# Kernel optimization log

Hardware: AMD Instinct MI355X
Metric: run time of the kernel (lower is better)

## Reference

```python
import math
import jax, jax.numpy as jnp
import numpy as np

B, S, HIDDEN = 1, 8192, 2048
NUM_HEADS = 16
HEAD_DIM = HIDDEN // NUM_HEADS
NUM_FW = 4
FW_DIM = HIDDEN // NUM_FW
D_H = FW_DIM  # inter_multi = 1.0
WINDOW = 256
CHUNK = 2048
ROPE_THETA = 500000.0
BASE_LR_INV = float(np.log(np.expm1(0.001)))  # inv_softplus(1e-3)


def rms_norm(x, w, eps=1e-6):
    return x * jax.lax.rsqrt(jnp.mean(x * x, axis=-1, keepdims=True) + eps) * w


def apply_rope(q, k, theta):
    D = q.shape[-1]
    inv = 1.0 / (theta ** (jnp.arange(0, D, 2, dtype=jnp.float32) / D))
    t = jnp.arange(q.shape[1], dtype=jnp.float32)
    f = t[:, None] * inv[None, :]  # [S, D/2]
    cos = jnp.cos(f)[None, :, None, :]
    sin = jnp.sin(f)[None, :, None, :]
    def ap(x):
        x1, x2 = jnp.split(x, 2, axis=-1)
        return jnp.concatenate([x1 * cos - x2 * sin, x2 * cos + x1 * sin], axis=-1)
    return ap(q), ap(k)


def sliding_window_attn(q, k, v, window):
    # q,k,v: [B,S,H,D]; causal window of `window` tokens incl. self (flash (window-1, 0))
    B_, S_, H_, D_ = q.shape
    W = window
    nc = S_ // W
    def blk(x):
        return x.transpose(0, 2, 1, 3).reshape(B_, H_, nc, W, D_)
    qb, kb, vb = blk(q), blk(k), blk(v)
    pad = jnp.zeros((B_, H_, 1, W, D_), q.dtype)
    k2 = jnp.concatenate([jnp.concatenate([pad, kb[:, :, :-1]], 2), kb], 3)  # [B,H,nc,2W,D]
    v2 = jnp.concatenate([jnp.concatenate([pad, vb[:, :, :-1]], 2), vb], 3)
    r = jnp.arange(W)[:, None]
    j = jnp.arange(2 * W)[None, :]
    base = (j >= r + 1) & (j <= W + r)  # causal + within-window
    keypos = (jnp.arange(nc)[:, None, None] - 1) * W + j[None]
    mask = base[None] & (keypos >= 0)  # [nc,W,2W]
    scores = jnp.einsum('bhnqd,bhnkd->bhnqk', qb, k2) * (1.0 / math.sqrt(D_))
    scores = jnp.where(mask[None, None], scores, -jnp.inf)
    p = jax.nn.softmax(scores, axis=-1)
    o = jnp.einsum('bhnqk,bhnkd->bhnqd', p, v2)
    return o.reshape(B_, H_, S_, D_).transpose(0, 2, 1, 3)


def ttt_swiglu(fq, fk, fv, l0, l1, l2, w0, w1, w2, chunk):
    # fq/fk/fv: [BN,S,d]; l*: [BN,S,1]; w0,w2: [BN,dh,d]; w1: [BN,d,dh]
    BN, S_, d = fq.shape
    nc = S_ // chunk
    def ch(x):
        return x.reshape(BN, nc, chunk, x.shape[-1]).transpose(1, 0, 2, 3)
    xs = (ch(fq), ch(fk), ch(fv), ch(l0), ch(l1), ch(l2))
    def step(carry, x):
        w0c, w1c, w2c = carry
        qi, ki, vi, lr0, lr1, lr2 = x
        # apply current fast weights to chunk queries (SwiGLU MLP)
        o = jnp.einsum('bch,boh->bco',
                       jax.nn.silu(jnp.einsum('bcd,bhd->bch', qi, w0c)) * jnp.einsum('bcd,bhd->bch', qi, w2c),
                       w1c)
        # manual gradient of dot-product TTT loss L = -sum(v * f(k))
        g = jnp.einsum('bcd,bhd->bch', ki, w0c)
        hm = jnp.einsum('bcd,bhd->bch', ki, w2c)
        sg = jax.nn.sigmoid(g)
        silu_g = g * sg
        hid = silu_g * hm
        dhid = jnp.einsum('bco,boh->bch', vi, w1c)
        dhm = dhid * silu_g
        dg = dhid * hm
        dgp = dg * (sg * (1.0 + g * (1.0 - sg)))  # silu backprop
        w0n = w0c + jnp.einsum('bch,bcd->bhd', dgp * lr0, ki)
        w2n = w2c + jnp.einsum('bch,bcd->bhd', dhm * lr2, ki)
        w1n = w1c + jnp.einsum('bco,bch->boh', vi * lr1, hid)
        return (w0n, w1n, w2n), o
    _, outs = jax.lax.scan(step, (w0, w1, w2), xs)
    return outs.transpose(1, 0, 2, 3).reshape(BN, S_, d)


def setup_inputs():
    key = jax.random.key(0)
    ks = jax.random.split(key, 8)
    h = HIDDEN
    return {
        'hidden_states': jax.random.normal(ks[0], (B, S, h), jnp.float32),
        'qkv_w': jax.random.normal(ks[1], (3 * h, h), jnp.float32) * 0.02,
        'q_norm_w': jnp.ones((h,), jnp.float32),
        'k_norm_w': jnp.ones((h,), jnp.float32),
        'qk_scale': jnp.ones((h, 2), jnp.float32),
        'qk_offset': jnp.zeros((h, 2), jnp.float32),
        'lr_w': jax.random.normal(ks[2], (3 * NUM_FW, h), jnp.float32) * 0.02,
        'lr_b': jnp.zeros((3 * NUM_FW,), jnp.float32),
        'w0': jax.random.normal(ks[3], (NUM_FW, D_H, FW_DIM), jnp.float32) / math.sqrt(FW_DIM),
        'w1': jax.random.normal(ks[4], (NUM_FW, FW_DIM, D_H), jnp.float32) / math.sqrt(D_H),
        'w2': jax.random.normal(ks[5], (NUM_FW, D_H, FW_DIM), jnp.float32) / math.sqrt(FW_DIM),
        'ttt_norm_w': jnp.ones((FW_DIM,), jnp.float32),
        'o_proj_w': jax.random.normal(ks[6], (h, h), jnp.float32) * 0.02,
    }


def reference(hidden_states, qkv_w, q_norm_w, k_norm_w, qk_scale, qk_offset,
              lr_w, lr_b, w0, w1, w2, ttt_norm_w, o_proj_w):
    qkv = hidden_states @ qkv_w.T
    q, k, v = jnp.split(qkv, 3, axis=-1)
    q = rms_norm(q, q_norm_w)
    k = rms_norm(k, k_norm_w)
    # rescale q/k for the fast-weight path
    fq = q * qk_scale[:, 0] + qk_offset[:, 0]
    fk = k * qk_scale[:, 1] + qk_offset[:, 1]
    fv = v
    # windowed RoPE attention path
    qh = q.reshape(B, S, NUM_HEADS, HEAD_DIM)
    kh = k.reshape(B, S, NUM_HEADS, HEAD_DIM)
    vh = v.reshape(B, S, NUM_HEADS, HEAD_DIM)
    qh, kh = apply_rope(qh, kh, ROPE_THETA)
    attn_o = sliding_window_attn(qh, kh, vh, WINDOW).reshape(B, S, HIDDEN)
    # fast-weight (TTT) path: silu + per-head l2-norm on q/k
    fq = jax.nn.silu(fq).reshape(B, S, NUM_FW, FW_DIM)
    fk = jax.nn.silu(fk).reshape(B, S, NUM_FW, FW_DIM)
    fv = jax.nn.silu(fv).reshape(B, S, NUM_FW, FW_DIM)
    fq = fq / jnp.maximum(jnp.linalg.norm(fq, axis=-1, keepdims=True), 1e-12)
    fk = fk / jnp.maximum(jnp.linalg.norm(fk, axis=-1, keepdims=True), 1e-12)
    def flat(x):
        return x.transpose(0, 2, 1, 3).reshape(B * NUM_FW, S, FW_DIM)
    # per-token learning rates (mamba parameterization)
    lr = jax.nn.softplus(hidden_states @ lr_w.T + lr_b + BASE_LR_INV)  # [B,S,3*NH]
    l0, l1, l2 = jnp.split(lr, 3, axis=-1)
    def flat_lr(x):
        return x.transpose(0, 2, 1).reshape(B * NUM_FW, S, 1)
    def bcast(w):
        return jnp.broadcast_to(w[None], (B,) + w.shape).reshape(B * NUM_FW, w.shape[1], w.shape[2])
    o_fast = ttt_swiglu(flat(fq), flat(fk), flat(fv),
                        flat_lr(l0), flat_lr(l1), flat_lr(l2),
                        bcast(w0), bcast(w1), bcast(w2), CHUNK)
    o_fast = rms_norm(o_fast.reshape(B, NUM_FW, S, FW_DIM), ttt_norm_w)
    o_fast = o_fast.transpose(0, 2, 1, 3).reshape(B, S, HIDDEN)
    return (attn_o + o_fast) @ o_proj_w.T
```

## Files before the change

### kernel.cpp

```cpp
#include <hip/hip_runtime.h>
#include <hip/hip_bf16.h>

typedef __hip_bfloat16 bf16;
typedef __bf16 bft;
typedef bft bf16x8 __attribute__((ext_vector_type(8)));
typedef bft bf16x4 __attribute__((ext_vector_type(4)));
typedef float f32x4 __attribute__((ext_vector_type(4)));

#define S_LEN 8192
#define HID   2048
#define QKV3  6144
#define NH    16
#define HD    128
#define NFW   4
#define FD    512
#define CHUNK_LEN 2048
#define NCHUNK 4
#define BASE_LR_INV (-6.9072552f)
#define QKP 136
#define VSP 72
#define PSP 76

__device__ __forceinline__ float bf2f(bf16 x){ return __bfloat162float(x); }
__device__ __forceinline__ bf16  f2bf(float x){ return __float2bfloat16(x); }
__device__ __forceinline__ float sigm(float x){ return 1.f/(1.f+__expf(-x)); }
__device__ __forceinline__ float siluf(float x){ return x/(1.f+__expf(-x)); }
__device__ __forceinline__ float wave_sum(float v){
  #pragma unroll
  for(int off=32; off; off>>=1) v += __shfl_xor(v, off, 64);
  return v;
}

template<int N>
__device__ __forceinline__ void waitcnt_vm(){
  static_assert(N==0||N==2||N==4||N==8, "unsupported vmcnt");
  if constexpr (N==0)      asm volatile("s_waitcnt vmcnt(0)" ::: "memory");
  else if constexpr (N==2) asm volatile("s_waitcnt vmcnt(2)" ::: "memory");
  else if constexpr (N==4) asm volatile("s_waitcnt vmcnt(4)" ::: "memory");
  else                     asm volatile("s_waitcnt vmcnt(8)" ::: "memory");
}

__device__ __forceinline__ void bar(){
  __builtin_amdgcn_s_barrier();
  asm volatile("" ::: "memory");
}

template<int ROWS>
__device__ __forceinline__ void stage(const bft* __restrict__ src, long ld,
                                      bft* dst, int tid)
{
  const int lane = tid & 63, wv = tid >> 6;
  #pragma unroll
  for (int i = 0; i < ROWS/64; ++i) {
    const int r0 = wv*16 + i*64;
    const int row = r0 + (lane >> 2);
    const int g = (lane & 3) ^ ((row >> 1) & 3);
    const bft* gp = src + (size_t)row*ld + g*8;
    bft* lp = dst + (size_t)r0*32;
    __builtin_amdgcn_global_load_lds(
        (const __attribute__((address_space(1))) void*)gp,
        (__attribute__((address_space(3))) void*)lp, 16, 0, 0);
  }
}

template<int BM,int BN,int EPI>
__global__ __launch_bounds__(256) void mgemm_k(
    const bft* __restrict__ A, const bft* __restrict__ B, void* __restrict__ Cv,
    bft* __restrict__ Cd, bft* __restrict__ Ct, int K,
    long lda, long ldb, long ldc, long sA, long sB, long sC, long sCd)
{
  constexpr int AM = BM/32, AN = BN/32;
  constexpr int LPT = BM/64 + BN/64;
  constexpr int NPH = (AM >= 4) ? 2 : 1;
  constexpr int MH  = AM / NPH;
  __shared__ __align__(16) bft As[4][BM*32];
  __shared__ __align__(16) bft Bs[4][BN*32];
  const int tid = threadIdx.x;
  const int z = blockIdx.z;
  A += (size_t)z * sA;
  B += (size_t)z * sB;
  const size_t m0 = (size_t)blockIdx.y * BM, n0 = (size_t)blockIdx.x * BN;
  const int wv = tid >> 6, lane = tid & 63;
  const int wm = (wv & 1) * (BM/2), wn = (wv >> 1) * (BN/2);
  const int fr = lane & 15;
  const int fsw = ((lane >> 4) ^ ((fr >> 1) & 3)) * 8;

  f32x4 acc[AM][AN];
  #pragma unroll
  for (int i=0;i<AM;i++)
    #pragma unroll
    for (int j=0;j<AN;j++) acc[i][j] = (f32x4){0.f,0.f,0.f,0.f};

  const bft* Ab = A + m0*lda;
  const bft* Bb = B + n0*ldb;
  const int NS = K >> 5;

  stage<BM>(Ab,      lda, As[0], tid);
  stage<BN>(Bb,      ldb, Bs[0], tid);
  stage<BM>(Ab + 32, lda, As[1], tid);
  stage<BN>(Bb + 32, ldb, Bs[1], tid);
  waitcnt_vm<LPT>();
  bar();

  for (int s = 0; s < NS; ++s) {
    const bft* Ap = As[s & 3];
    const bft* Bp = Bs[s & 3];
    const int kt = (s + 2) * 32;
    const bool st = (s + 2 < NS);

    bf16x8 bvv[AN], afv[MH];
    #pragma unroll
    for (int ni=0; ni<AN; ni++)
      bvv[ni] = *(const bf16x8*)(Bp + (size_t)(wn + ni*16 + fr)*32 + fsw);
    #pragma unroll
    for (int i=0; i<MH; i++)
      afv[i] = *(const bf16x8*)(Ap + (size_t)(wm + i*16 + fr)*32 + fsw);
    if (st) stage<BM>(Ab + kt, lda, As[(s+2)&3], tid);
    if constexpr (NPH == 1) {
      if (st) { stage<BN>(Bb + kt, ldb, Bs[(s+2)&3], tid); waitcnt_vm<LPT>(); }
      else waitcnt_vm<0>();
    }
    bar();
    __builtin_amdgcn_s_setprio(1);
    #pragma unroll
    for (int i=0; i<MH; i++)
      #pragma unroll
      for (int ni=0; ni<AN; ni++)
        acc[i][ni] = __builtin_amdgcn_mfma_f32_16x16x32_bf16(afv[i], bvv[ni], acc[i][ni], 0, 0, 0);
    __builtin_amdgcn_s_setprio(0);

    if constexpr (NPH == 2) {
      bar();
      #pragma unroll
      for (int i=0; i<MH; i++)
        afv[i] = *(const bf16x8*)(Ap + (size_t)(wm + (MH+i)*16 + fr)*32 + fsw);
      if (st) { stage<BN>(Bb + kt, ldb, Bs[(s+2)&3], tid); waitcnt_vm<LPT>(); }
      else waitcnt_vm<0>();
      bar();
      __builtin_amdgcn_s_setprio(1);
      #pragma unroll
      for (int i=0; i<MH; i++)
        #pragma unroll
        for (int ni=0; ni<AN; ni++)
          acc[MH+i][ni] = __builtin_amdgcn_mfma_f32_16x16x32_bf16(afv[i], bvv[ni], acc[MH+i][ni], 0, 0, 0);
      __builtin_amdgcn_s_setprio(0);
      bar();
    }
  }

  const int er = (lane >> 4) * 4;
  const int ec = lane & 15;
  #pragma unroll
  for (int mi=0; mi<AM; mi++){
    #pragma unroll
    for (int ni=0; ni<AN; ni++){
      #pragma unroll
      for (int r=0; r<4; r++){
        size_t row = m0 + wm + mi*16 + er + r;
        size_t col = n0 + wn + ni*16 + ec;
        size_t idx = (size_t)z*sC + row*ldc + col;
        float v = acc[mi][ni][r];
        if constexpr (EPI == 0){
          ((bft*)Cv)[idx] = (bft)v;
        } else if constexpr (EPI == 1){
          ((float*)Cv)[idx] = v;
        } else {
          float nv = ((float*)Cv)[idx] + v;
          ((float*)Cv)[idx] = nv;
          Cd[(size_t)z*sCd + row*ldc + col] = (bft)nv;
          if (Ct) Ct[(size_t)z*FD*FD + col*FD + row] = (bft)nv;
        }
      }
    }
  }
}

template<int BM,int BN,int EPI>
static inline void mgemm(hipStream_t st, const bft* A, const bft* B, void* C,
    bft* Cd, bft* Ct, int M, int N, int K, long lda, long ldb, long ldc,
    int batch, long sA, long sB, long sC, long sCd)
{
  dim3 g(N/BN, M/BM, batch);
  mgemm_k<BM,BN,EPI><<<g, 256, 0, st>>>(A, B, C, Cd, Ct, K, lda, ldb, ldc, sA, sB, sC, sCd);
}

__device__ __forceinline__ void stage8(const bft* __restrict__ src, long ld,
                                       bft* dst, int tid)
{
  const int lane = tid & 63, wv = tid >> 6;
  #pragma unroll
  for (int i = 0; i < 2; ++i) {
    const int r0 = wv*16 + i*128;
    const int row = r0 + (lane >> 2);
    const int g = (lane & 3) ^ ((row >> 1) & 3);
    const bft* gp = src + (size_t)row*ld + g*8;
    bft* lp = dst + (size_t)r0*32;
    __builtin_amdgcn_global_load_lds(
        (const __attribute__((address_space(1))) void*)gp,
        (__attribute__((address_space(3))) void*)lp, 16, 0, 0);
  }
}

#define M8_ROW(mi, a) { \
    acc[mi][0]=__builtin_amdgcn_mfma_f32_16x16x32_bf16(a,bv[0],acc[mi][0],0,0,0); \
    acc[mi][1]=__builtin_amdgcn_mfma_f32_16x16x32_bf16(a,bv[1],acc[mi][1],0,0,0); \
    acc[mi][2]=__builtin_amdgcn_mfma_f32_16x16x32_bf16(a,bv[2],acc[mi][2],0,0,0); \
    acc[mi][3]=__builtin_amdgcn_mfma_f32_16x16x32_bf16(a,bv[3],acc[mi][3],0,0,0); }

template<int EPI>
__global__ __launch_bounds__(512, 2) void mgemm8_k(
    const bft* __restrict__ A, const bft* __restrict__ B, void* __restrict__ Cv,
    int K, long lda, long ldb, long ldc)
{
  __shared__ __align__(16) bft As[4][256*32];
  __shared__ __align__(16) bft Bs[4][256*32];
  const int tid = threadIdx.x;

  const int gx = (int)gridDim.x;
  const int nwg = (int)(gridDim.x * gridDim.y);
  int lin = (int)(blockIdx.y * gridDim.x + blockIdx.x);
  if ((nwg & 7) == 0) lin = (lin & 7) * (nwg >> 3) + (lin >> 3);
  const size_t m0 = (size_t)(lin / gx) * 256;
  const size_t n0 = (size_t)(lin % gx) * 256;

  const int wv = tid >> 6, lane = tid & 63;
  const int wm = (wv & 1) * 128, wn = (wv >> 1) * 64;
  const int fr = lane & 15;
  const int fsw = ((lane >> 4) ^ ((fr >> 1) & 3)) * 8;

  f32x4 acc[8][4];
  #pragma unroll
  for (int i=0;i<8;i++)
    #pragma unroll
    for (int j=0;j<4;j++) acc[i][j] = (f32x4){0.f,0.f,0.f,0.f};

  const bft* Ab = A + m0*lda;
  const bft* Bb = B + n0*ldb;
  const int NS = K >> 5;

  stage8(Ab,      lda, As[0], tid);
  stage8(Bb,      ldb, Bs[0], tid);
  stage8(Ab + 32, lda, As[1], tid);
  stage8(Bb + 32, ldb, Bs[1], tid);
  waitcnt_vm<4>();
  bar();

  for (int s = 0; s < NS; ++s) {
    const bft* Ap = As[s & 3];
    const bft* Bp = Bs[s & 3];
    const int kt = (s + 2) * 32;
    const bool st = (s + 2 < NS);
    bf16x8 bv[4], a0, a1, a2, a3;

    bv[0] = *(const bf16x8*)(Bp + (size_t)(wn +  0 + fr)*32 + fsw);
    bv[1] = *(const bf16x8*)(Bp + (size_t)(wn + 16 + fr)*32 + fsw);
    bv[2] = *(const bf16x8*)(Bp + (size_t)(wn + 32 + fr)*32 + fsw);
    bv[3] = *(const bf16x8*)(Bp + (size_t)(wn + 48 + fr)*32 + fsw);
    a0 = *(const bf16x8*)(Ap + (size_t)(wm +  0 + fr)*32 + fsw);
    a1 = *(const bf16x8*)(Ap + (size_t)(wm + 16 + fr)*32 + fsw);
    a2 = *(const bf16x8*)(Ap + (size_t)(wm + 32 + fr)*32 + fsw);
    a3 = *(const bf16x8*)(Ap + (size_t)(wm + 48 + fr)*32 + fsw);
    if (st) stage8(Ab + kt, lda, As[(s+2)&3], tid);
    bar();
    __builtin_amdgcn_s_setprio(1);
    M8_ROW(0, a0); M8_ROW(1, a1); M8_ROW(2, a2); M8_ROW(3, a3);
    __builtin_amdgcn_s_setprio(0);
    bar();

    a0 = *(const bf16x8*)(Ap + (size_t)(wm +  64 + fr)*32 + fsw);
    a1 = *(const bf16x8*)(Ap + (size_t)(wm +  80 + fr)*32 + fsw);
    a2 = *(const bf16x8*)(Ap + (size_t)(wm +  96 + fr)*32 + fsw);
    a3 = *(const bf16x8*)(Ap + (size_t)(wm + 112 + fr)*32 + fsw);
    if (st) { stage8(Bb + kt, ldb, Bs[(s+2)&3], tid); waitcnt_vm<4>(); }
    else waitcnt_vm<0>();
    bar();
    __builtin_amdgcn_s_setprio(1);
    M8_ROW(4, a0); M8_ROW(5, a1); M8_ROW(6, a2); M8_ROW(7, a3);
    __builtin_amdgcn_s_setprio(0);
    bar();
  }

  const int er = (lane >> 4) * 4;
  const int ec = lane & 15;
  #pragma unroll
  for (int mi=0; mi<8; mi++){
    #pragma unroll
    for (int ni=0; ni<4; ni++){
      #pragma unroll
      for (int r=0; r<4; r++){
        size_t row = m0 + wm + mi*16 + er + r;
        size_t col = n0 + wn + ni*16 + ec;
        size_t idx = row*ldc + col;
        float v = acc[mi][ni][r];
        if constexpr (EPI == 0) ((bft*)Cv)[idx] = (bft)v;
        else                    ((float*)Cv)[idx] = v;
      }
    }
  }
}

template<int EPI>
static inline void mgemm8(hipStream_t st, const bft* A, const bft* B, void* C,
                          int M, int N, int K, long lda, long ldb, long ldc)
{
  dim3 g(N/256, M/256, 1);
  mgemm8_k<EPI><<<g, 512, 0, st>>>(A, B, C, K, lda, ldb, ldc);
}

__global__ __launch_bounds__(256) void cvt_k(const float* __restrict__ s,
    bft* __restrict__ d)
{
  size_t i = ((size_t)blockIdx.x*256 + threadIdx.x) * 8;
  const float4 v0 = *(const float4*)(s + i);
  const float4 v1 = *(const float4*)(s + i + 4);
  bf16x8 b;
  b[0]=(bft)v0.x; b[1]=(bft)v0.y; b[2]=(bft)v0.z; b[3]=(bft)v0.w;
  b[4]=(bft)v1.x; b[5]=(bft)v1.y; b[6]=(bft)v1.z; b[7]=(bft)v1.w;
  *(bf16x8*)(d + i) = b;
}

__global__ __launch_bounds__(256) void tr_k(const bft* __restrict__ in,
    bft* __restrict__ out, long ldin, long sIn, long sOut)
{
  __shared__ __align__(16) bft t[64][72];
  const int c0 = blockIdx.x*64, r0 = blockIdx.y*64;
  in  += (size_t)blockIdx.z * sIn;
  out += (size_t)blockIdx.z * sOut;
  const int tid = threadIdx.x;
  #pragma unroll
  for (int i=0;i<2;i++){
    int e = tid + i*256;
    int r = e >> 3, c8 = (e & 7) * 8;
    *(bf16x8*)&t[r][c8] = *(const bf16x8*)(in + (size_t)(r0+r)*ldin + c0 + c8);
  }
  __syncthreads();
  #pragma unroll
  for (int i=0;i<2;i++){
    int e = tid + i*256;
    int c = e >> 3, r8 = (e & 7) * 8;
    bf16x8 v;
    #pragma unroll
    for (int j=0;j<8;j++) v[j] = t[r8+j][c];
    *(bf16x8*)(out + (size_t)(c0+c)*CHUNK_LEN + r0 + r8) = v;
  }
}

__global__ __launch_bounds__(256) void tcw1_k(const float* __restrict__ w1,
    bft* __restrict__ w1tb)
{
  size_t idx = (size_t)blockIdx.x*256 + threadIdx.x;
  int z = (int)(idx >> 18);
  int h = (int)((idx >> 9) & 511);
  int o = (int)(idx & 511);
  w1tb[idx] = (bft)w1[(size_t)z*FD*FD + (size_t)o*FD + h];
}

__global__ __launch_bounds__(256) void vt_k(const bf16* __restrict__ qkv,
    bft* __restrict__ vT)
{
  __shared__ __align__(16) bft t[64*QKP];
  const int s0 = blockIdx.x * 64;
  const int h  = blockIdx.y;
  const int tid = threadIdx.x;
  #pragma unroll
  for (int i=0;i<4;i++){
    int e = tid + i*256;
    int rr = e >> 4, doff = (e & 15) * 8;
    *(bf16x8*)(t + rr*QKP + doff) =
        *(const bf16x8*)((const bft*)qkv + (size_t)(s0+rr)*QKV3 + 2*HID + h*HD + doff);
  }
  __syncthreads();
  #pragma unroll
  for (int it=0; it<4; it++){
    int d = (tid >> 3) + it*32;
    int so8 = (tid & 7) * 8;
    bf16x8 v;
    #pragma unroll
    for (int j=0;j<8;j++) v[j] = t[(so8+j)*QKP + d];
    *(bf16x8*)(vT + ((size_t)(h*HD + d))*S_LEN + s0 + so8) = v;
  }
}

__global__ void rope_k(float* __restrict__ rc, float* __restrict__ rs){
  int pos = blockIdx.x, d = threadIdx.x;
  float inv = 1.f / powf(500000.0f, (float)d * (1.0f/64.0f));
  float ang = (float)pos * inv;
  rc[pos*64+d] = cosf(ang);
  rs[pos*64+d] = sinf(ang);
}

__global__ __launch_bounds__(256) void lr_k(const float* __restrict__ hidden,
    const float* __restrict__ lr_w, const float* __restrict__ lr_b,
    float* __restrict__ lro)
{
  __shared__ float hrow[HID];
  __shared__ float red[4][12];
  int s = blockIdx.x, tid = threadIdx.x;
  for(int i=0;i<HID/256;i++) hrow[tid+256*i] = hidden[(size_t)s*HID + tid + 256*i];
  __syncthreads();
  float part[12];
  #pragma unroll
  for(int o=0;o<12;o++) part[o]=0.f;
  for(int i=0;i<HID/256;i++){
    int j = tid + 256*i;
    float h = hrow[j];
    #pragma unroll
    for(int o=0;o<12;o++) part[o] += h * lr_w[o*HID + j];
  }
  int lane = tid & 63, w = tid >> 6;
  #pragma unroll
  for(int o=0;o<12;o++){
    float v = wave_sum(part[o]);
    if(lane==0) red[w][o] = v;
  }
  __syncthreads();
  if(tid < 12){
    float v = red[0][tid]+red[1][tid]+red[2][tid]+red[3][tid] + lr_b[tid] + BASE_LR_INV;
    float sp = (v > 20.f) ? v : log1pf(expf(v));
    lro[s*12 + tid] = sp;
  }
}

__global__ __launch_bounds__(256) void e2a_k(
    bf16* __restrict__ qkv,
    const float* __restrict__ qnw, const float* __restrict__ knw)
{
  __shared__ float red[8];
  int s = blockIdx.x, tid = threadIdx.x;
  int lane = tid & 63, w = tid >> 6;
  float qv[8], kv[8];
  float sq = 0.f, sk = 0.f;
  size_t base = (size_t)s*QKV3;
  #pragma unroll
  for(int i=0;i<8;i++){
    int j = tid*8 + i;
    qv[i] = bf2f(qkv[base + j]);
    kv[i] = bf2f(qkv[base + HID + j]);
    sq += qv[i]*qv[i]; sk += kv[i]*kv[i];
  }
  sq = wave_sum(sq); sk = wave_sum(sk);
  if(lane==0){ red[w] = sq; red[4+w] = sk; }
  __syncthreads();
  float rq = rsqrtf((red[0]+red[1]+red[2]+red[3])*(1.f/HID) + 1e-6f);
  float rk = rsqrtf((red[4]+red[5]+red[6]+red[7])*(1.f/HID) + 1e-6f);
  #pragma unroll
  for(int i=0;i<8;i++){
    int j = tid*8 + i;
    qkv[base + j]       = f2bf(qv[i]*rq*qnw[j]);
    qkv[base + HID + j] = f2bf(kv[i]*rk*knw[j]);
  }
}

__global__ __launch_bounds__(256) void e2b_k(
    bf16* __restrict__ qkv,
    const float* __restrict__ qks, const float* __restrict__ qko)
{
  int s = blockIdx.x, tid = threadIdx.x;
  size_t base = (size_t)s*QKV3;
  float a[8], b[8], vv[8];
  float ga = 0.f, gb2 = 0.f;
  #pragma unroll
  for(int i=0;i<8;i++){
    int j = tid*8 + i;
    float qn = bf2f(qkv[base + j]);
    float kn = bf2f(qkv[base + HID + j]);
    float v  = bf2f(qkv[base + 2*HID + j]);
    a[i] = siluf(qn*qks[2*j]   + qko[2*j]);
    b[i] = siluf(kn*qks[2*j+1] + qko[2*j+1]);
    vv[i] = siluf(v);
    ga += a[i]*a[i]; gb2 += b[i]*b[i];
  }
  ga = wave_sum(ga); gb2 = wave_sum(gb2);
  float iq = 1.f / fmaxf(sqrtf(ga), 1e-12f);
  float ik = 1.f / fmaxf(sqrtf(gb2), 1e-12f);
  #pragma unroll
  for(int i=0;i<8;i++){
    int j = tid*8 + i;
    qkv[base + j]         = f2bf(a[i]*iq);
    qkv[base + HID + j]   = f2bf(b[i]*ik);
    qkv[base + 2*HID + j] = f2bf(vv[i]);
  }
}

__global__ __launch_bounds__(256) void attn_k(
    const bf16* __restrict__ qkv, const bft* __restrict__ vT,
    const float* __restrict__ rc, const float* __restrict__ rs,
    float* __restrict__ attn)
{
  __shared__ __align__(16) bft Qs[64*QKP];
  __shared__ __align__(16) bft Ks[64*QKP];
  __shared__ __align__(16) bft Vs[128*VSP];
  __shared__ __align__(16) bft Ps[64*PSP];
  const int head = blockIdx.x >> 7;
  const int Q0 = (blockIdx.x & 127) * 64;
  const int tid = threadIdx.x;
  const int hb = head * HD;
  const int lane = tid & 63;
  const int wm = (tid >> 6) * 16;
  const int fr = lane & 15, fko = (lane >> 4) * 8;
  const int rbase = (lane >> 4) * 4;

  #pragma unroll
  for(int i=0;i<16;i++){
    int e = tid + i*256;
    int rr = e >> 6, d = e & 63;
    int qpos = Q0 + rr;
    size_t b = (size_t)qpos*QKV3 + hb;
    float x1 = bf2f(qkv[b + d]);
    float x2 = bf2f(qkv[b + d + 64]);
    float c = rc[qpos*64 + d], sn = rs[qpos*64 + d];
    Qs[rr*QKP + d]      = (bft)(x1*c - x2*sn);
    Qs[rr*QKP + d + 64] = (bft)(x2*c + x1*sn);
  }
  __syncthreads();
  bf16x8 qf[4];
  #pragma unroll
  for (int kk=0;kk<4;kk++)
    qf[kk] = *(const bf16x8*)(Qs + (wm+fr)*QKP + kk*32 + fko);

  f32x4 Ot[8];
  #pragma unroll
  for (int i=0;i<8;i++) Ot[i] = (f32x4){0.f,0.f,0.f,0.f};
  float m4[4], l4[4];
  #pragma unroll
  for (int r=0;r<4;r++){ m4[r] = -INFINITY; l4[r] = 0.f; }

  for (int kt=0; kt<5; kt++){
    const int kb = Q0 - 256 + kt*64;
    if (kb < 0) continue;
    __syncthreads();
    #pragma unroll
    for(int i=0;i<16;i++){
      int e = tid + i*256;
      int rr = e >> 6, d = e & 63;
      int kpos = kb + rr;
      size_t b = (size_t)kpos*QKV3 + HID + hb;
      float x1 = bf2f(qkv[b + d]);
      float x2 = bf2f(qkv[b + d + 64]);
      float c = rc[kpos*64 + d], sn = rs[kpos*64 + d];
      Ks[rr*QKP + d]      = (bft)(x1*c - x2*sn);
      Ks[rr*QKP + d + 64] = (bft)(x2*c + x1*sn);
    }
    {
      int d = tid >> 1, koff = (tid & 1) * 32;
      const bft* vrow = vT + ((size_t)(hb + d))*S_LEN + kb + koff;
      bft* lrow = Vs + d*VSP + koff;
      #pragma unroll
      for (int j8=0;j8<4;j8++)
        *(bf16x8*)(lrow + j8*8) = *(const bf16x8*)(vrow + j8*8);
    }
    __syncthreads();

    f32x4 st[4];
    #pragma unroll
    for (int nt=0;nt<4;nt++){
      f32x4 acc = (f32x4){0.f,0.f,0.f,0.f};
      #pragma unroll
      for (int kk=0;kk<4;kk++){
        bf16x8 kf = *(const bf16x8*)(Ks + (nt*16+fr)*QKP + kk*32 + fko);
        acc = __builtin_amdgcn_mfma_f32_16x16x32_bf16(qf[kk], kf, acc, 0, 0, 0);
      }
      st[nt] = acc;
    }

    float pv[4][4];
    #pragma unroll
    for (int r=0;r<4;r++){
      int qpos = Q0 + wm + rbase + r;
      float sm[4];
      float mx = -INFINITY;
      #pragma unroll
      for (int nt=0;nt<4;nt++){
        int kpos = kb + nt*16 + fr;
        bool valid = (kpos > qpos - 256) && (kpos <= qpos);
        float s = valid ? st[nt][r] * 0.088388347648318447f : -INFINITY;
        sm[nt] = s;
        mx = fmaxf(mx, s);
      }
      mx = fmaxf(mx, __shfl_xor(mx, 1, 64));
      mx = fmaxf(mx, __shfl_xor(mx, 2, 64));
      mx = fmaxf(mx, __shfl_xor(mx, 4, 64));
      mx = fmaxf(mx, __shfl_xor(mx, 8, 64));
      float mnew = fmaxf(m4[r], mx);
      float alpha = (mnew == -INFINITY) ? 1.f : __expf(m4[r] - mnew);
      float ps = 0.f;
      #pragma unroll
      for (int nt=0;nt<4;nt++){
        float p = (sm[nt] == -INFINITY) ? 0.f : __expf(sm[nt] - mnew);
        pv[nt][r] = p;
        ps += p;
      }
      ps += __shfl_xor(ps, 1, 64);
      ps += __shfl_xor(ps, 2, 64);
      ps += __shfl_xor(ps, 4, 64);
      ps += __shfl_xor(ps, 8, 64);
      l4[r] = l4[r]*alpha + ps;
      m4[r] = mnew;
      #pragma unroll
      for (int ct=0;ct<8;ct++) Ot[ct][r] *= alpha;
    }

    #pragma unroll
    for (int r=0;r<4;r++){
      int row = wm + rbase + r;
      #pragma unroll
      for (int nt=0;nt<4;nt++)
        Ps[row*PSP + nt*16 + fr] = (bft)pv[nt][r];
    }
    bf16x8 af[2];
    #pragma unroll
    for (int kk=0;kk<2;kk++){
      const bft* pp = Ps + (wm+fr)*PSP + kk*32 + fko;
      bf16x4 lo = *(const bf16x4*)pp;
      bf16x4 hi = *(const bf16x4*)(pp+4);
      bf16x8 a;
      #pragma unroll
      for (int j=0;j<4;j++){ a[j]=lo[j]; a[j+4]=hi[j]; }
      af[kk]=a;
    }
    #pragma unroll
    for (int ct=0;ct<8;ct++)
      #pragma unroll
      for (int kk=0;kk<2;kk++){
        bf16x8 bv = *(const bf16x8*)(Vs + (ct*16+fr)*VSP + kk*32 + fko);
        Ot[ct] = __builtin_amdgcn_mfma_f32_16x16x32_bf16(af[kk], bv, Ot[ct], 0, 0, 0);
      }
  }

  #pragma unroll
  for (int r=0;r<4;r++){
    float invl = 1.f / l4[r];
    int qpos = Q0 + wm + rbase + r;
    size_t ob = (size_t)qpos*HID + hb;
    #pragma unroll
    for (int ct=0;ct<8;ct++)
      attn[ob + ct*16 + fr] = Ot[ct][r] * invl;
  }
}

__global__ __launch_bounds__(256) void e3f_k(
    bft* __restrict__ gh, bft* __restrict__ qgm, bft* __restrict__ hid)
{
  size_t idx = (size_t)blockIdx.x*256 + threadIdx.x;
  int z  = (int)(idx >> 20);
  int ci = (int)((idx >> 9) & 2047);
  int d  = (int)(idx & 511);
  size_t b = ((size_t)z*CHUNK_LEN + ci)*1024 + d;
  float opre = siluf((float)qgm[b]) * (float)qgm[b + 512];
  hid[idx] = (bft)(siluf((float)gh[b]) * (float)gh[b + 512]);
  qgm[b]   = (bft)opre;
}

__global__ __launch_bounds__(256) void e4f_k(
    bft* __restrict__ gh, bft* __restrict__ qgm,
    const bf16* __restrict__ qkv, const float* __restrict__ lrb, int cbase)
{
  size_t idx = (size_t)blockIdx.x*256 + threadIdx.x;
  int z  = (int)(idx >> 20);
  int ci = (int)((idx >> 9) & 2047);
  int d  = (int)(idx & 511);
  int s  = cbase + ci;
  float l0  = lrb[s*12 + z];
  float l1  = lrb[s*12 + 4 + z];
  float l2v = lrb[s*12 + 8 + z];
  size_t b = ((size_t)z*CHUNK_LEN + ci)*1024 + d;
  float gg = (float)gh[b], hv = (float)gh[b + 512], dh = (float)qgm[b + 512];
  float sg = sigm(gg);
  float silu_g = gg * sg;
  float dhm = dh * silu_g;
  float dg  = dh * hv;
  float dgp = dg * (sg * (1.f + gg * (1.f - sg)));
  float fvv = bf2f(qkv[(size_t)s*QKV3 + 2*HID + z*FD + d]);
  gh[b]        = (bft)(dgp * l0);
  gh[b + 512]  = (bft)(dhm * l2v);
  qgm[b + 512] = (bft)(fvv * l1);
}

__global__ __launch_bounds__(256) void e5_k(const float* __restrict__ attn,
    const bf16* __restrict__ ofc, const float* __restrict__ tnw,
    bf16* __restrict__ qkv, int cbase)
{
  int ci = blockIdx.x, tid = threadIdx.x;
  int s = cbase + ci;
  int lane = tid & 63, w = tid >> 6;
  float o[8]; float ss = 0.f;
  size_t ob = ((size_t)w*CHUNK_LEN + ci)*FD + (size_t)lane*8;
  #pragma unroll
  for(int i=0;i<8;i++){ o[i] = bf2f(ofc[ob+i]); ss += o[i]*o[i]; }
  ss = wave_sum(ss);
  float inv = rsqrtf(ss*(1.f/FD) + 1e-6f);
  size_t xb = (size_t)s*QKV3 + w*FD + (size_t)lane*8;
  size_t ab = (size_t)s*HID  + w*FD + (size_t)lane*8;
  #pragma unroll
  for(int i=0;i<8;i++){
    int d = lane*8 + i;
    qkv[xb+i] = f2bf(attn[ab+i] + o[i]*inv*tnw[d]);
  }
}

extern "C" void kernel_launch(void* const* d_in, const int* in_sizes, int n_in,
                              void* d_out, int out_size, void* d_ws, size_t ws_size,
                              hipStream_t stream)
{
  (void)in_sizes; (void)n_in; (void)out_size;
  const float* hidden   = (const float*)d_in[0];
  const float* qkv_w    = (const float*)d_in[1];
  const float* q_norm_w = (const float*)d_in[2];
  const float* k_norm_w = (const float*)d_in[3];
  const float* qk_scale = (const float*)d_in[4];
  const float* qk_off   = (const float*)d_in[5];
  const float* lr_w     = (const float*)d_in[6];
  const float* lr_b     = (const float*)d_in[7];
  const float* w0_in    = (const float*)d_in[8];
  const float* w1_in    = (const float*)d_in[9];
  const float* w2_in    = (const float*)d_in[10];
  const float* ttt_nw   = (const float*)d_in[11];
  const float* o_proj   = (const float*)d_in[12];
  float* out = (float*)d_out;

  char* p = (char*)d_ws;
  auto alloc = [&](size_t n){ char* r = p; p += (n + 255) & ~(size_t)255; return (void*)r; };

  bf16*  qkv   = (bf16*) alloc((size_t)S_LEN*QKV3*sizeof(bf16));
  float* lrb   = (float*)alloc((size_t)S_LEN*12*sizeof(float));
  float* rc    = (float*)alloc((size_t)S_LEN*64*sizeof(float));
  float* rs    = (float*)alloc((size_t)S_LEN*64*sizeof(float));
  float* w0s   = (float*)alloc((size_t)NFW*FD*FD*sizeof(float));
  float* w1s   = (float*)alloc((size_t)NFW*FD*FD*sizeof(float));
  float* w2s   = (float*)alloc((size_t)NFW*FD*FD*sizeof(float));
  bft*   w1tb  = (bft*)  alloc((size_t)NFW*FD*FD*sizeof(bft));
  bft*   w02b  = (bft*)  alloc((size_t)NFW*1024*FD*sizeof(bft));
  bft*   w1b   = (bft*)  alloc((size_t)NFW*FD*FD*sizeof(bft));
  bf16*  gb    = (bf16*) alloc((size_t)NFW*CHUNK_LEN*FD*sizeof(bf16));
  bf16*  hmb   = (bf16*) alloc((size_t)NFW*CHUNK_LEN*FD*sizeof(bf16));
  bf16*  qgb   = (bf16*) alloc((size_t)NFW*CHUNK_LEN*FD*sizeof(bf16));
  bf16*  qmb   = (bf16*) alloc((size_t)NFW*CHUNK_LEN*FD*sizeof(bf16));
  bf16*  hidb  = (bf16*) alloc((size_t)NFW*CHUNK_LEN*FD*sizeof(bf16));
  bf16*  ofc   = (bf16*) alloc((size_t)NFW*CHUNK_LEN*FD*sizeof(bf16));
  bft*   fkT   = (bft*)  alloc((size_t)NFW*FD*CHUNK_LEN*sizeof(bft));
  bft*   hidT  = (bft*)  alloc((size_t)NFW*FD*CHUNK_LEN*sizeof(bft));
  bft*   a2T   = (bft*)  alloc((size_t)NFW*FD*CHUNK_LEN*sizeof(bft));

  if ((size_t)(p - (char*)d_ws) > ws_size) return;

  bft* ghb = (bft*)gb;
  bft* qgm = (bft*)qgb;
  bft* hidden_bf = (bft*)gb;
  bft* qkvw_bf   = (bft*)fkT;
  bft* vT        = (bft*)fkT;
  bft* opw_bf    = (bft*)hidb;

  float* attn = out;

  const long sW  = (long)FD*FD;
  const long sW2 = (long)1024*FD;
  const long sCh = (long)CHUNK_LEN*FD;
  const long sGH = (long)CHUNK_LEN*1024;
  const long sT  = (long)FD*CHUNK_LEN;

  hipMemcpyAsync(w0s, w0_in, (size_t)NFW*FD*FD*sizeof(float), hipMemcpyDeviceToDevice, stream);
  hipMemcpyAsync(w1s, w1_in, (size_t)NFW*FD*FD*sizeof(float), hipMemcpyDeviceToDevice, stream);
  hipMemcpyAsync(w2s, w2_in, (size_t)NFW*FD*FD*sizeof(float), hipMemcpyDeviceToDevice, stream);

  rope_k<<<S_LEN, 64, 0, stream>>>(rc, rs);
  lr_k<<<S_LEN, 256, 0, stream>>>(hidden, lr_w, lr_b, lrb);
  tcw1_k<<<NFW*FD*FD/256, 256, 0, stream>>>(w1_in, w1tb);
  cvt_k<<<(NFW*FD*FD)/2048, 256, 0, stream>>>(w1_in, w1b);
  for (int z = 0; z < NFW; ++z) {
    cvt_k<<<(FD*FD)/2048, 256, 0, stream>>>(w0_in + (size_t)z*sW, w02b + (size_t)z*sW2);
    cvt_k<<<(FD*FD)/2048, 256, 0, stream>>>(w2_in + (size_t)z*sW, w02b + (size_t)z*sW2 + (size_t)512*FD);
  }
  cvt_k<<<(S_LEN*HID)/2048, 256, 0, stream>>>(hidden, hidden_bf);
  cvt_k<<<(QKV3*HID)/2048, 256, 0, stream>>>(qkv_w, qkvw_bf);

  mgemm8<0>(stream, hidden_bf, qkvw_bf, (void*)qkv, S_LEN, QKV3, HID, HID, HID, QKV3);

  e2a_k<<<S_LEN, 256, 0, stream>>>(qkv, q_norm_w, k_norm_w);
  vt_k<<<dim3(S_LEN/64, NH), 256, 0, stream>>>(qkv, vT);
  attn_k<<<NH*128, 256, 0, stream>>>(qkv, vT, rc, rs, attn);
  e2b_k<<<S_LEN, 256, 0, stream>>>(qkv, qk_scale, qk_off);

  const int  NEL = NFW*CHUNK_LEN*FD/256;
  const dim3 tg(FD/64, CHUNK_LEN/64, NFW);

  for(int c=0; c<NCHUNK; c++){
    const bft* fqc = (const bft*)qkv + (size_t)c*CHUNK_LEN*QKV3;
    const bft* fkc = fqc + HID;
    const bft* fvc = fqc + 2*HID;
    mgemm<128,128,0>(stream, fkc, w02b, ghb, nullptr, nullptr,
        CHUNK_LEN, 1024, FD, QKV3, FD, 1024, NFW, FD, sW2, sGH, 0);
    mgemm<128,128,0>(stream, fqc, w02b, qgm, nullptr, nullptr,
        CHUNK_LEN, 1024, FD, QKV3, FD, 1024, NFW, FD, sW2, sGH, 0);
    e3f_k<<<NEL, 256, 0, stream>>>(ghb, qgm, (bft*)hidb);
    mgemm<128,128,0>(stream, (const bft*)qgm, w1b, ofc, nullptr, nullptr,
        CHUNK_LEN, FD, FD, 1024, FD, FD, NFW, sGH, sW, sCh, 0);
    mgemm<128,128,0>(stream, fvc, (const bft*)w1tb, qgm + 512, nullptr, nullptr,
        CHUNK_LEN, FD, FD, QKV3, FD, 1024, NFW, FD, sW, sGH, 0);
    e4f_k<<<NEL, 256, 0, stream>>>(ghb, qgm, qkv, lrb, c*CHUNK_LEN);
    tr_k<<<tg, 256, 0, stream>>>(fkc,              fkT,  QKV3, FD,  sT);
    tr_k<<<tg, 256, 0, stream>>>((const bft*)hidb, hidT, FD,   sCh, sT);
    tr_k<<<tg, 256, 0, stream>>>(ghb,       a2T, 1024, sGH, sT);
    mgemm<64,64,2>(stream, a2T, fkT,  w0s, w02b, nullptr,
        FD, FD, CHUNK_LEN, CHUNK_LEN, CHUNK_LEN, FD, NFW, sT, sT, sW, sW2);
    tr_k<<<tg, 256, 0, stream>>>(ghb + 512, a2T, 1024, sGH, sT);
    mgemm<64,64,2>(stream, a2T, fkT,  w2s, w02b + (size_t)512*FD, nullptr,
        FD, FD, CHUNK_LEN, CHUNK_LEN, CHUNK_LEN, FD, NFW, sT, sT, sW, sW2);
    tr_k<<<tg, 256, 0, stream>>>(qgm + 512, a2T, 1024, sGH, sT);
    mgemm<64,64,2>(stream, a2T, hidT, w1s, w1b, w1tb,
        FD, FD, CHUNK_LEN, CHUNK_LEN, CHUNK_LEN, FD, NFW, sT, sT, sW, sW);
    e5_k<<<CHUNK_LEN, 256, 0, stream>>>(attn, ofc, ttt_nw, qkv, c*CHUNK_LEN);
  }

  cvt_k<<<(HID*HID)/2048, 256, 0, stream>>>(o_proj, opw_bf);
  mgemm8<1>(stream, (const bft*)qkv, opw_bf, out, S_LEN, HID, HID, QKV3, HID, HID);
}
```

Measured before the change: 1.507 ms.

## Double-buffer MFMA register fragments to overlap LDS reads with matrix math

```diff
diff --git a/kernel.cpp b/kernel.cpp
--- a/kernel.cpp
+++ b/kernel.cpp
@@ -71,8 +71,6 @@
 {
   constexpr int AM = BM/32, AN = BN/32;
   constexpr int LPT = BM/64 + BN/64;
-  constexpr int NPH = (AM >= 4) ? 2 : 1;
-  constexpr int MH  = AM / NPH;
   __shared__ __align__(16) bft As[4][BM*32];
   __shared__ __align__(16) bft Bs[4][BN*32];
   const int tid = threadIdx.x;
@@ -102,50 +100,47 @@
   waitcnt_vm<LPT>();
   bar();
 
-  for (int s = 0; s < NS; ++s) {
-    const bft* Ap = As[s & 3];
-    const bft* Bp = Bs[s & 3];
+  bf16x8 aP[AM], bP[AN], aQ[AM], bQ[AN];
+  #pragma unroll
+  for (int mi=0; mi<AM; mi++)
+    aP[mi] = *(const bf16x8*)(As[0] + (size_t)(wm + mi*16 + fr)*32 + fsw);
+  #pragma unroll
+  for (int ni=0; ni<AN; ni++)
+    bP[ni] = *(const bf16x8*)(Bs[0] + (size_t)(wn + ni*16 + fr)*32 + fsw);
+
+  auto body = [&](bf16x8 (&ac)[AM], bf16x8 (&bc)[AN],
+                  bf16x8 (&an)[AM], bf16x8 (&bn)[AN], int s){
     const int kt = (s + 2) * 32;
-    const bool st = (s + 2 < NS);
-
-    bf16x8 bvv[AN], afv[MH];
-    #pragma unroll
-    for (int ni=0; ni<AN; ni++)
-      bvv[ni] = *(const bf16x8*)(Bp + (size_t)(wn + ni*16 + fr)*32 + fsw);
-    #pragma unroll
-    for (int i=0; i<MH; i++)
-      afv[i] = *(const bf16x8*)(Ap + (size_t)(wm + i*16 + fr)*32 + fsw);
-    if (st) stage<BM>(Ab + kt, lda, As[(s+2)&3], tid);
-    if constexpr (NPH == 1) {
-      if (st) { stage<BN>(Bb + kt, ldb, Bs[(s+2)&3], tid); waitcnt_vm<LPT>(); }
-      else waitcnt_vm<0>();
-    }
-    bar();
+    const bool st2 = (s + 2 < NS);
+    const bool rd  = (s + 1 < NS);
+    if (st2) {
+      stage<BM>(Ab + kt, lda, As[(s+2)&3], tid);
+      stage<BN>(Bb + kt, ldb, Bs[(s+2)&3], tid);
+    }
+    if (rd) {
+      if (st2) waitcnt_vm<LPT>(); else waitcnt_vm<0>();
+      bar();
+      const bft* An = As[(s+1)&3];
+      const bft* Bn = Bs[(s+1)&3];
+      #pragma unroll
+      for (int mi=0; mi<AM; mi++)
+        an[mi] = *(const bf16x8*)(An + (size_t)(wm + mi*16 + fr)*32 + fsw);
+      #pragma unroll
+      for (int ni=0; ni<AN; ni++)
+        bn[ni] = *(const bf16x8*)(Bn + (size_t)(wn + ni*16 + fr)*32 + fsw);
+    }
     __builtin_amdgcn_s_setprio(1);
     #pragma unroll
-    for (int i=0; i<MH; i++)
+    for (int mi=0; mi<AM; mi++)
       #pragma unroll
       for (int ni=0; ni<AN; ni++)
-        acc[i][ni] = __builtin_amdgcn_mfma_f32_16x16x32_bf16(afv[i], bvv[ni], acc[i][ni], 0, 0, 0);
+        acc[mi][ni] = __builtin_amdgcn_mfma_f32_16x16x32_bf16(ac[mi], bc[ni], acc[mi][ni], 0, 0, 0);
     __builtin_amdgcn_s_setprio(0);
-
-    if constexpr (NPH == 2) {
-      bar();
-      #pragma unroll
-      for (int i=0; i<MH; i++)
-        afv[i] = *(const bf16x8*)(Ap + (size_t)(wm + (MH+i)*16 + fr)*32 + fsw);
-      if (st) { stage<BN>(Bb + kt, ldb, Bs[(s+2)&3], tid); waitcnt_vm<LPT>(); }
-      else waitcnt_vm<0>();
-      bar();
-      __builtin_amdgcn_s_setprio(1);
-      #pragma unroll
-      for (int i=0; i<MH; i++)
-        #pragma unroll
-        for (int ni=0; ni<AN; ni++)
-          acc[MH+i][ni] = __builtin_amdgcn_mfma_f32_16x16x32_bf16(afv[i], bvv[ni], acc[MH+i][ni], 0, 0, 0);
-      __builtin_amdgcn_s_setprio(0);
-      bar();
-    }
+  };
+
+  for (int s = 0; s < NS; s += 2) {
+    body(aP, bP, aQ, bQ, s);
+    body(aQ, bQ, aP, bP, s + 1);
   }
 
   const int er = (lane >> 4) * 4;
@@ -201,12 +196,6 @@
   }
 }
 
-#define M8_ROW(mi, a) { \
-    acc[mi][0]=__builtin_amdgcn_mfma_f32_16x16x32_bf16(a,bv[0],acc[mi][0],0,0,0); \
-    acc[mi][1]=__builtin_amdgcn_mfma_f32_16x16x32_bf16(a,bv[1],acc[mi][1],0,0,0); \
-    acc[mi][2]=__builtin_amdgcn_mfma_f32_16x16x32_bf16(a,bv[2],acc[mi][2],0,0,0); \
-    acc[mi][3]=__builtin_amdgcn_mfma_f32_16x16x32_bf16(a,bv[3],acc[mi][3],0,0,0); }
-
 template<int EPI>
 __global__ __launch_bounds__(512, 2) void mgemm8_k(
     const bft* __restrict__ A, const bft* __restrict__ B, void* __restrict__ Cv,
@@ -245,39 +234,47 @@
   waitcnt_vm<4>();
   bar();
 
-  for (int s = 0; s < NS; ++s) {
-    const bft* Ap = As[s & 3];
-    const bft* Bp = Bs[s & 3];
+  bf16x8 aP[8], bP[4], aQ[8], bQ[4];
+  #pragma unroll
+  for (int mi=0; mi<8; mi++)
+    aP[mi] = *(const bf16x8*)(As[0] + (size_t)(wm + mi*16 + fr)*32 + fsw);
+  #pragma unroll
+  for (int ni=0; ni<4; ni++)
+    bP[ni] = *(const bf16x8*)(Bs[0] + (size_t)(wn + ni*16 + fr)*32 + fsw);
+
+  auto body = [&](bf16x8 (&ac)[8], bf16x8 (&bc)[4],
+                  bf16x8 (&an)[8], bf16x8 (&bn)[4], int s){
     const int kt = (s + 2) * 32;
-    const bool st = (s + 2 < NS);
-    bf16x8 bv[4], a0, a1, a2, a3;
-
-    bv[0] = *(const bf16x8*)(Bp + (size_t)(wn +  0 + fr)*32 + fsw);
-    bv[1] = *(const bf16x8*)(Bp + (size_t)(wn + 16 + fr)*32 + fsw);
-    bv[2] = *(const bf16x8*)(Bp + (size_t)(wn + 32 + fr)*32 + fsw);
-    bv[3] = *(const bf16x8*)(Bp + (size_t)(wn + 48 + fr)*32 + fsw);
-    a0 = *(const bf16x8*)(Ap + (size_t)(wm +  0 + fr)*32 + fsw);
-    a1 = *(const bf16x8*)(Ap + (size_t)(wm + 16 + fr)*32 + fsw);
-    a2 = *(const bf16x8*)(Ap + (size_t)(wm + 32 + fr)*32 + fsw);
-    a3 = *(const bf16x8*)(Ap + (size_t)(wm + 48 + fr)*32 + fsw);
-    if (st) stage8(Ab + kt, lda, As[(s+2)&3], tid);
-    bar();
+    const bool st2 = (s + 2 < NS);
+    const bool rd  = (s + 1 < NS);
+    if (st2) {
+      stage8(Ab + kt, lda, As[(s+2)&3], tid);
+      stage8(Bb + kt, ldb, Bs[(s+2)&3], tid);
+    }
+    if (rd) {
+      if (st2) waitcnt_vm<4>(); else waitcnt_vm<0>();
+      bar();
+      const bft* An = As[(s+1)&3];
+      const bft* Bn = Bs[(s+1)&3];
+      #pragma unroll
+      for (int mi=0; mi<8; mi++)
+        an[mi] = *(const bf16x8*)(An + (size_t)(wm + mi*16 + fr)*32 + fsw);
+      #pragma unroll
+      for (int ni=0; ni<4; ni++)
+        bn[ni] = *(const bf16x8*)(Bn + (size_t)(wn + ni*16 + fr)*32 + fsw);
+    }
     __builtin_amdgcn_s_setprio(1);
-    M8_ROW(0, a0); M8_ROW(1, a1); M8_ROW(2, a2); M8_ROW(3, a3);
+    #pragma unroll
+    for (int mi=0; mi<8; mi++)
+      #pragma unroll
+      for (int ni=0; ni<4; ni++)
+        acc[mi][ni] = __builtin_amdgcn_mfma_f32_16x16x32_bf16(ac[mi], bc[ni], acc[mi][ni], 0, 0, 0);
     __builtin_amdgcn_s_setprio(0);
-    bar();
-
-    a0 = *(const bf16x8*)(Ap + (size_t)(wm +  64 + fr)*32 + fsw);
-    a1 = *(const bf16x8*)(Ap + (size_t)(wm +  80 + fr)*32 + fsw);
-    a2 = *(const bf16x8*)(Ap + (size_t)(wm +  96 + fr)*32 + fsw);
-    a3 = *(const bf16x8*)(Ap + (size_t)(wm + 112 + fr)*32 + fsw);
-    if (st) { stage8(Bb + kt, ldb, Bs[(s+2)&3], tid); waitcnt_vm<4>(); }
-    else waitcnt_vm<0>();
-    bar();
-    __builtin_amdgcn_s_setprio(1);
-    M8_ROW(4, a0); M8_ROW(5, a1); M8_ROW(6, a2); M8_ROW(7, a3);
-    __builtin_amdgcn_s_setprio(0);
-    bar();
+  };
+
+  for (int s = 0; s < NS; s += 2) {
+    body(aP, bP, aQ, bQ, s);
+    body(aQ, bQ, aP, bP, s + 1);
   }
 
   const int er = (lane >> 4) * 4;
```

New measurement: 1.506 ms. Within noise of the previous version (-0.0%).
